# Optimization experiments

Hardware: AMD Instinct MI355X
Metric: run time of the kernel (lower is better)

The kernel has to match this reference:

```python
import jax, jax.numpy as jnp
import numpy as np

B, S, D, H = 4, 2048, 1024, 16
DEPTH = D // H
NEG = float(-2**32 + 1)


def setup_inputs() -> dict:
    key = jax.random.key(0)
    ks = jax.random.split(key, 9)
    std = 1.0 / np.sqrt(D)
    return {
        "q": jax.random.normal(ks[0], (B, S, D), jnp.float32),
        "k": jax.random.normal(ks[1], (B, S, D), jnp.float32),
        "v": jax.random.normal(ks[2], (B, S, D), jnp.float32),
        "Wq": jax.random.normal(ks[3], (D, D), jnp.float32) * std,
        "bq": jnp.zeros((D,), jnp.float32),
        "Wk": jax.random.normal(ks[4], (D, D), jnp.float32) * std,
        "bk": jnp.zeros((D,), jnp.float32),
        "Wv": jax.random.normal(ks[5], (D, D), jnp.float32) * std,
        "bv": jnp.zeros((D,), jnp.float32),
    }


def _split_heads(x):
    # (B,S,D) -> head-major (H*B, S, depth), matching tf stack-on-axis0
    return x.reshape(B, S, H, DEPTH).transpose(2, 0, 1, 3).reshape(H * B, S, DEPTH)


def _merge_heads(x):
    # (H*B, S, depth) -> (B, S, D), heads concatenated on feature dim
    return x.reshape(H, B, S, DEPTH).transpose(1, 2, 0, 3).reshape(B, S, D)


def _attention(qh, kh, vh):
    scale = 1.0 / jnp.sqrt(jnp.float32(DEPTH))
    scores = jnp.einsum("nsd,ntd->nst", qh, kh) * scale  # (N,S,S)
    key_mask = jnp.sign(jnp.abs(jnp.sum(kh, axis=-1)))    # (N,S)
    scores = jnp.where(key_mask[:, None, :] == 0, NEG, scores)
    tril = jnp.tril(jnp.ones((S, S), jnp.float32))
    scores = jnp.where(tril[None] == 0, NEG, scores)
    attn = jax.nn.softmax(scores, axis=-1)
    query_mask = jnp.sign(jnp.abs(jnp.sum(qh, axis=-1)))   # (N,S)
    attn = attn * query_mask[:, :, None]
    return jnp.einsum("nst,ntd->nsd", attn, vh)


def reference(q, k, v, Wq, bq, Wk, bk, Wv, bv):
    qh = _split_heads(q @ Wq + bq)
    kh = _split_heads(k @ Wk + bk)
    vh = _split_heads(v @ Wv + bv)
    out = _attention(qh, kh, vh)
    return _merge_heads(out)
```

## Files before the change

kernel.cpp:

```cpp
#include <hip/hip_runtime.h>

#define S_LEN   2048
#define D_MODEL 1024
#define NB      4
#define NH      16
#define DEP     64
#define NHEADS  64
#define M_ROWS  8192

typedef __bf16 bf16_t;
typedef bf16_t bf16x8 __attribute__((ext_vector_type(8)));
typedef bf16_t bf16x2 __attribute__((ext_vector_type(2)));
typedef float  f32x4  __attribute__((ext_vector_type(4)));
typedef float  f32x16 __attribute__((ext_vector_type(16)));
typedef unsigned int u32x4 __attribute__((ext_vector_type(4)));

#define LOG2E 1.4426950408889634f
#define QSCALE 0.18033688011112043f

#if __has_builtin(__builtin_amdgcn_exp2f)
  #define EXP2(x) __builtin_amdgcn_exp2f(x)
#else
  #define EXP2(x) exp2f(x)
#endif

#define GLOBAL_AS(p) ((const __attribute__((address_space(1))) void*)(p))
#define LDS_AS(p)    ((__attribute__((address_space(3))) void*)(p))

__device__ __forceinline__ unsigned short bf16r(float f) {
  unsigned u = __builtin_bit_cast(unsigned, f);
  u = (u + 0x7FFFu + ((u >> 16) & 1u)) >> 16;
  return (unsigned short)u;
}

__device__ __forceinline__ unsigned pkbf(float lo, float hi) {
  bf16x2 t;
  t[0] = (bf16_t)lo;
  t[1] = (bf16_t)hi;
  return __builtin_bit_cast(unsigned, t);
}

__device__ __forceinline__ bf16x8 exppack8(
    float a0, float a1, float a2, float a3,
    float a4, float a5, float a6, float a7, float& ssum) {
  float e0 = EXP2(a0);
  float e1 = EXP2(a1);
  float e2 = EXP2(a2);
  float e3 = EXP2(a3);
  float e4 = EXP2(a4);
  float e5 = EXP2(a5);
  float e6 = EXP2(a6);
  float e7 = EXP2(a7);
  ssum += ((e0 + e1) + (e2 + e3)) + ((e4 + e5) + (e6 + e7));
  u32x4 fw = {pkbf(e0, e1), pkbf(e2, e3), pkbf(e4, e5), pkbf(e6, e7)};
  return __builtin_bit_cast(bf16x8, fw);
}

__global__ __launch_bounds__(256) void transpose_cvt_w3(
    const float* __restrict__ Wq, const float* __restrict__ Wk,
    const float* __restrict__ Wv,
    unsigned short* __restrict__ oq, unsigned short* __restrict__ ok,
    unsigned short* __restrict__ ov) {
  __shared__ unsigned short tile[32][33];
  int z = blockIdx.z;
  const float* in = (z == 0) ? Wq : (z == 1) ? Wk : Wv;
  unsigned short* out = (z == 0) ? oq : (z == 1) ? ok : ov;
  int bx = blockIdx.x * 32;
  int by = blockIdx.y * 32;
  int tx = threadIdx.x & 31, ty = threadIdx.x >> 5;
  for (int i = ty; i < 32; i += 8)
    tile[i][tx] = bf16r(in[(by + i) * D_MODEL + bx + tx]);
  __syncthreads();
  for (int i = ty; i < 32; i += 8)
    out[(size_t)(bx + i) * D_MODEL + by + tx] = tile[tx][i];
}

__global__ __launch_bounds__(256, 3) void gemm_qkv3(
    const float* __restrict__ Aq, const float* __restrict__ Ak,
    const float* __restrict__ Av,
    const unsigned short* __restrict__ Btq, const unsigned short* __restrict__ Btk,
    const unsigned short* __restrict__ Btv,
    const float* __restrict__ bq, const float* __restrict__ bk,
    const float* __restrict__ bv,
    unsigned short* __restrict__ oq, unsigned short* __restrict__ ok,
    unsigned short* __restrict__ ov) {
  __shared__ __align__(16) float          Asb[128 * 64];
  __shared__ __align__(16) unsigned short Bsb[128 * 64];
  int z = blockIdx.z;
  const float* A           = (z == 0) ? Aq  : (z == 1) ? Ak  : Av;
  const unsigned short* Bt = (z == 0) ? Btq : (z == 1) ? Btk : Btv;
  const float* bias        = (z == 0) ? bq  : (z == 1) ? bk  : bv;
  unsigned short* out      = (z == 0) ? oq  : (z == 1) ? ok  : ov;
  const float scale        = (z == 0) ? QSCALE : 1.0f;
  int tid = threadIdx.x, lane = tid & 63, wid = tid >> 6;
  int lr = lane & 15, lg = lane >> 4;
  int m0 = blockIdx.x * 128, n0 = blockIdx.y * 128;
  int wr = wid >> 1, wc = wid & 1;
  f32x4 acc[4][4] = {};
  for (int kt = 0; kt < D_MODEL / 64; kt++) {
    int k0 = kt * 64;
    if (kt) __syncthreads();
#pragma unroll
    for (int i = 0; i < 8; i++) {
      int chunk = i * 256 + tid;
      int row = chunk >> 4, c = chunk & 15;
      int csrc = c ^ (row & 7);
      __builtin_amdgcn_global_load_lds(
          GLOBAL_AS(A + (size_t)(m0 + row) * D_MODEL + k0 + csrc * 4),
          LDS_AS(Asb + (size_t)(i * 256 + wid * 64) * 4), 16, 0, 0);
    }
#pragma unroll
    for (int i = 0; i < 4; i++) {
      int chunk = i * 256 + tid;
      int r = chunk >> 3, c = chunk & 7;
      int csrc = c ^ (r & 7);
      __builtin_amdgcn_global_load_lds(
          GLOBAL_AS(Bt + (size_t)(n0 + r) * D_MODEL + k0 + csrc * 8),
          LDS_AS(Bsb + (size_t)(i * 256 + wid * 64) * 8), 16, 0, 0);
    }
    __syncthreads();
#pragma unroll
    for (int ks = 0; ks < 2; ks++) {
      bf16x8 af[4], bfr[4];
#pragma unroll
      for (int mi = 0; mi < 4; mi++) {
        int row = wr * 64 + mi * 16 + lr;
        int c0 = (ks * 8 + lg * 2) ^ (row & 7);
        int c1 = (ks * 8 + lg * 2 + 1) ^ (row & 7);
        f32x4 a0 = *(const f32x4*)(Asb + row * 64 + c0 * 4);
        f32x4 a1 = *(const f32x4*)(Asb + row * 64 + c1 * 4);
        u32x4 w = {pkbf(a0[0], a0[1]), pkbf(a0[2], a0[3]),
                   pkbf(a1[0], a1[1]), pkbf(a1[2], a1[3])};
        af[mi] = __builtin_bit_cast(bf16x8, w);
      }
#pragma unroll
      for (int ni = 0; ni < 4; ni++) {
        int row = wc * 64 + ni * 16 + lr;
        int c = (ks * 4 + lg) ^ (row & 7);
        bfr[ni] = *(const bf16x8*)(Bsb + row * 64 + c * 8);
      }
#pragma unroll
      for (int mi = 0; mi < 4; mi++)
#pragma unroll
        for (int ni = 0; ni < 4; ni++)
          acc[mi][ni] = __builtin_amdgcn_mfma_f32_16x16x32_bf16(
              af[mi], bfr[ni], acc[mi][ni], 0, 0, 0);
    }
  }
  if (z != 2) {
#pragma unroll
    for (int mi = 0; mi < 4; mi++) {
#pragma unroll
      for (int ni = 0; ni < 4; ni++) {
        int col = n0 + wc * 64 + ni * 16 + lr;
        float bvv = bias[col];
        int h = col >> 6, d = col & 63;
#pragma unroll
        for (int r = 0; r < 4; r++) {
          int row = m0 + wr * 64 + mi * 16 + lg * 4 + r;
          int b = row >> 11, s = row & (S_LEN - 1);
          float val = (acc[mi][ni][r] + bvv) * scale;
          out[((size_t)(h * NB + b) * S_LEN + s) * DEP + d] = bf16r(val);
        }
      }
    }
  } else {
    int sadj_off = (lg == 1) ? 4 : (lg == 2) ? -4 : 0;
#pragma unroll
    for (int mi = 0; mi < 4; mi++) {
#pragma unroll
      for (int ni = 0; ni < 4; ni++) {
        int col = n0 + wc * 64 + ni * 16 + lr;
        float bvv = bias[col];
        int row0 = m0 + wr * 64 + mi * 16 + lg * 4;
        int b = row0 >> 11, s = (row0 & (S_LEN - 1)) + sadj_off;
        ushort4 w;
        w.x = bf16r(acc[mi][ni][0] + bvv);
        w.y = bf16r(acc[mi][ni][1] + bvv);
        w.z = bf16r(acc[mi][ni][2] + bvv);
        w.w = bf16r(acc[mi][ni][3] + bvv);
        *(ushort4*)(out + ((size_t)((col >> 6) * NB + b) * DEP + (col & 63)) * S_LEN + s) = w;
      }
    }
  }
}

__global__ __launch_bounds__(256, 2) void attn_fwd(
    const unsigned short* __restrict__ Q,
    const unsigned short* __restrict__ K,
    const unsigned short* __restrict__ Vt,
    float* __restrict__ out) {
  __shared__ __align__(16) char smem[65536];
  const int tid = threadIdx.x, lane = tid & 63, wid = tid >> 6;
  const int l31 = lane & 31, hi = lane >> 5;
  const int id = blockIdx.x;
  const int xcd = id & 7, hh = (id >> 3) & 7, u = id >> 6;
  const int n = xcd * 8 + hh;
  const int h = n >> 2, b = n & 3;
  const unsigned short* Qh = Q + (size_t)n * S_LEN * DEP;
  const unsigned short* Kh = K + (size_t)n * S_LEN * DEP;
  const unsigned short* Vh = Vt + (size_t)n * DEP * S_LEN;
  const int S31 = (l31 & 7) << 4;
  const int scol = ((lane & 7) ^ (lane >> 3)) * 8;
  const int srow = lane >> 3;

#define STAGE_TILE(kvb, bi)                                                   \
  {                                                                           \
    char* base_ = smem + (bi) * 16384;                                        \
    const unsigned short* ksrc =                                              \
        Kh + (size_t)((kvb) + wid * 16 + srow) * DEP + scol;                  \
    const unsigned short* vsrc =                                              \
        Vh + (size_t)(wid * 16 + srow) * S_LEN + (kvb) + scol;                \
    unsigned short* kdst = (unsigned short*)base_ + wid * 16 * 64;            \
    unsigned short* vdst = (unsigned short*)(base_ + 8192) + wid * 16 * 64;   \
    __builtin_amdgcn_global_load_lds(GLOBAL_AS(ksrc), LDS_AS(kdst), 16, 0, 0);\
    __builtin_amdgcn_global_load_lds(GLOBAL_AS(ksrc + 8 * DEP),               \
                                     LDS_AS(kdst + 8 * 64), 16, 0, 0);        \
    __builtin_amdgcn_global_load_lds(GLOBAL_AS(vsrc), LDS_AS(vdst), 16, 0, 0);\
    __builtin_amdgcn_global_load_lds(GLOBAL_AS(vsrc + 8 * S_LEN),             \
                                     LDS_AS(vdst + 8 * 64), 16, 0, 0);        \
  }

  for (int pass = 0; pass < 2; ++pass) {
    const int j = pass ? 63 - (u * 4 + wid) : u * 4 + wid;
    const int nt_w = (j >> 1) + 1;
    const int nt_blk = pass ? 32 - 2 * u : 2 * u + 2;
    const int q0 = j * 32;
    const int qrow = q0 + l31;

    bf16x8 qf[4];
#pragma unroll
    for (int ds = 0; ds < 4; ds++)
      qf[ds] = *(const bf16x8*)(Qh + (size_t)qrow * DEP + ds * 16 + hi * 8);

    f32x16 o0 = {}, o1 = {};
    float l = 0.f;

    __syncthreads();
    STAGE_TILE(0, 0);
    STAGE_TILE(64, 1);

    for (int t = 0; t < nt_blk; ++t) {
      if (t + 2 < nt_blk) {
        STAGE_TILE((t + 2) * 64, (t + 2) & 3);
        asm volatile("s_waitcnt vmcnt(8)" ::: "memory");
      } else if (t + 1 < nt_blk) {
        asm volatile("s_waitcnt vmcnt(4)" ::: "memory");
      } else {
        asm volatile("s_waitcnt vmcnt(0)" ::: "memory");
      }
      __builtin_amdgcn_s_barrier();
      asm volatile("" ::: "memory");
      if (t < nt_w) {
        const char* kb = smem + (t & 3) * 16384;
        const char* vb = kb + 8192;
        const int kvb = t * 64;
        const bool diag = (t == nt_w - 1);
        float ssum = 0.f;

        {
          f32x16 p0 = {};
          __builtin_amdgcn_s_setprio(1);
#pragma unroll
          for (int ds = 0; ds < 4; ds++) {
            int off = (ds * 32 + hi * 16) ^ S31;
            bf16x8 kf = *(const bf16x8*)(kb + l31 * 128 + off);
            p0 = __builtin_amdgcn_mfma_f32_32x32x16_bf16(kf, qf[ds], p0, 0, 0, 0);
          }
          __builtin_amdgcn_s_setprio(0);
          if (diag) {
#pragma unroll
            for (int r = 0; r < 16; r++) {
              int kvr = kvb + (r & 3) + 8 * (r >> 2) + 4 * hi;
              if (kvr > qrow) p0[r] = -3.0e38f;
            }
          }
          bf16x8 pa0 = exppack8(p0[0], p0[1], p0[2], p0[3],
                                p0[4], p0[5], p0[6], p0[7], ssum);
          bf16x8 pa1 = exppack8(p0[8], p0[9], p0[10], p0[11],
                                p0[12], p0[13], p0[14], p0[15], ssum);
          __builtin_amdgcn_s_setprio(1);
          {
            int off0 = (0 * 32 + hi * 16) ^ S31;
            int off1 = (1 * 32 + hi * 16) ^ S31;
            bf16x8 vfa = *(const bf16x8*)(vb + l31 * 128 + off0);
            bf16x8 vfb = *(const bf16x8*)(vb + (l31 + 32) * 128 + off0);
            o0 = __builtin_amdgcn_mfma_f32_32x32x16_bf16(vfa, pa0, o0, 0, 0, 0);
            o1 = __builtin_amdgcn_mfma_f32_32x32x16_bf16(vfb, pa0, o1, 0, 0, 0);
            bf16x8 vfc = *(const bf16x8*)(vb + l31 * 128 + off1);
            bf16x8 vfd = *(const bf16x8*)(vb + (l31 + 32) * 128 + off1);
            o0 = __builtin_amdgcn_mfma_f32_32x32x16_bf16(vfc, pa1, o0, 0, 0, 0);
            o1 = __builtin_amdgcn_mfma_f32_32x32x16_bf16(vfd, pa1, o1, 0, 0, 0);
          }
          __builtin_amdgcn_s_setprio(0);
        }
        {
          f32x16 p1 = {};
          __builtin_amdgcn_s_setprio(1);
#pragma unroll
          for (int ds = 0; ds < 4; ds++) {
            int off = (ds * 32 + hi * 16) ^ S31;
            bf16x8 kf = *(const bf16x8*)(kb + (l31 + 32) * 128 + off);
            p1 = __builtin_amdgcn_mfma_f32_32x32x16_bf16(kf, qf[ds], p1, 0, 0, 0);
          }
          __builtin_amdgcn_s_setprio(0);
          if (diag) {
#pragma unroll
            for (int r = 0; r < 16; r++) {
              int kvr = kvb + 32 + (r & 3) + 8 * (r >> 2) + 4 * hi;
              if (kvr > qrow) p1[r] = -3.0e38f;
            }
          }
          bf16x8 pa2 = exppack8(p1[0], p1[1], p1[2], p1[3],
                                p1[4], p1[5], p1[6], p1[7], ssum);
          bf16x8 pa3 = exppack8(p1[8], p1[9], p1[10], p1[11],
                                p1[12], p1[13], p1[14], p1[15], ssum);
          __builtin_amdgcn_s_setprio(1);
          {
            int off0 = (2 * 32 + hi * 16) ^ S31;
            int off1 = (3 * 32 + hi * 16) ^ S31;
            bf16x8 vfa = *(const bf16x8*)(vb + l31 * 128 + off0);
            bf16x8 vfb = *(const bf16x8*)(vb + (l31 + 32) * 128 + off0);
            o0 = __builtin_amdgcn_mfma_f32_32x32x16_bf16(vfa, pa2, o0, 0, 0, 0);
            o1 = __builtin_amdgcn_mfma_f32_32x32x16_bf16(vfb, pa2, o1, 0, 0, 0);
            bf16x8 vfc = *(const bf16x8*)(vb + l31 * 128 + off1);
            bf16x8 vfd = *(const bf16x8*)(vb + (l31 + 32) * 128 + off1);
            o0 = __builtin_amdgcn_mfma_f32_32x32x16_bf16(vfc, pa3, o0, 0, 0, 0);
            o1 = __builtin_amdgcn_mfma_f32_32x32x16_bf16(vfd, pa3, o1, 0, 0, 0);
          }
          __builtin_amdgcn_s_setprio(0);
        }
        ssum += __shfl_xor(ssum, 32);
        l += ssum;
      }
    }
    __syncthreads();

    const float inv = 1.0f / l;
    float* ow = (float*)(smem + wid * 8192);
    const int es = (l31 & 7) << 2;
#pragma unroll
    for (int r = 0; r < 16; r++) {
      int d0 = (r & 3) + 8 * (r >> 2) + 4 * hi;
      ow[l31 * 64 + (d0 ^ es)]        = o0[r] * inv;
      ow[l31 * 64 + ((d0 + 32) ^ es)] = o1[r] * inv;
    }
    asm volatile("s_waitcnt lgkmcnt(0)" ::: "memory");
    __builtin_amdgcn_sched_barrier(0);
#pragma unroll
    for (int i = 0; i < 8; i++) {
      int idx = i * 64 + lane;
      int row = idx >> 4;
      int c4 = idx & 15;
      float4 vv = *(const float4*)&ow[row * 64 + ((c4 * 4) ^ ((row & 7) << 2))];
      *(float4*)(out + (size_t)(b * S_LEN + q0 + row) * D_MODEL + h * DEP + c4 * 4) = vv;
    }
  }
#undef STAGE_TILE
}

extern "C" void kernel_launch(void* const* d_in, const int* in_sizes, int n_in,
                              void* d_out, int out_size, void* d_ws, size_t ws_size,
                              hipStream_t stream) {
  const float* q  = (const float*)d_in[0];
  const float* k  = (const float*)d_in[1];
  const float* v  = (const float*)d_in[2];
  const float* Wq = (const float*)d_in[3];
  const float* bq = (const float*)d_in[4];
  const float* Wk = (const float*)d_in[5];
  const float* bk = (const float*)d_in[6];
  const float* Wv = (const float*)d_in[7];
  const float* bv = (const float*)d_in[8];
  float* out = (float*)d_out;

  const size_t WN = (size_t)D_MODEL * D_MODEL;
  const size_t HN = (size_t)NHEADS * S_LEN * DEP;

  unsigned short* Qh  = (unsigned short*)d_ws;
  unsigned short* Kh  = Qh + HN;
  unsigned short* Vts = Kh + HN;
  unsigned short* Wqt = Vts + HN;
  unsigned short* Wkt = Wqt + WN;
  unsigned short* Wvt = Wkt + WN;

  transpose_cvt_w3<<<dim3(32, 32, 3), 256, 0, stream>>>(Wq, Wk, Wv, Wqt, Wkt, Wvt);

  gemm_qkv3<<<dim3(M_ROWS / 128, D_MODEL / 128, 3), 256, 0, stream>>>(
      q, k, v, Wqt, Wkt, Wvt, bq, bk, bv, Qh, Kh, Vts);

  attn_fwd<<<1024, 256, 0, stream>>>(Qh, Kh, Vts, out);
}
```

Baseline: 175.0 us.

## Process 64 query rows per wave to reuse staged K/V tiles

Each wave now handles two 32-row query sub-blocks (64 rows) instead of one, so every K and V fragment read from LDS feeds twice as many MFMAs. The grid is halved to 512 blocks and the causal diagonal handling skips the fully masked quarter. The aim is to cut LDS read traffic and staging overhead per unit of work. In exchange it raises register pressure (two Q fragment sets and four accumulators), which may lower occupancy, and leaves fewer blocks for load balancing.

```diff
diff --git a/kernel.cpp b/kernel.cpp
--- a/kernel.cpp
+++ b/kernel.cpp
@@ -221,20 +221,84 @@
                                      LDS_AS(vdst + 8 * 64), 16, 0, 0);        \
   }
 
+#define DO_HALF(KROW, VKS, qfv, o0v, o1v, ssumv, qrowv, domask)               \
+  {                                                                           \
+    f32x16 p = {};                                                            \
+    __builtin_amdgcn_s_setprio(1);                                            \
+    _Pragma("unroll")                                                         \
+    for (int ds = 0; ds < 4; ds++) {                                          \
+      int off = (ds * 32 + hi * 16) ^ S31;                                    \
+      bf16x8 kf = *(const bf16x8*)(kb + (l31 + (KROW)) * 128 + off);          \
+      p = __builtin_amdgcn_mfma_f32_32x32x16_bf16(kf, qfv[ds], p, 0, 0, 0);   \
+    }                                                                         \
+    __builtin_amdgcn_s_setprio(0);                                            \
+    if (domask) {                                                             \
+      _Pragma("unroll")                                                       \
+      for (int r = 0; r < 16; r++) {                                          \
+        int kvr = kvb + (KROW) + (r & 3) + 8 * (r >> 2) + 4 * hi;             \
+        if (kvr > (qrowv)) p[r] = -3.0e38f;                                   \
+      }                                                                       \
+    }                                                                         \
+    bf16x8 paA_ = exppack8(p[0], p[1], p[2], p[3],                            \
+                           p[4], p[5], p[6], p[7], ssumv);                    \
+    bf16x8 paB_ = exppack8(p[8], p[9], p[10], p[11],                          \
+                           p[12], p[13], p[14], p[15], ssumv);                \
+    __builtin_amdgcn_s_setprio(1);                                            \
+    {                                                                         \
+      int off0 = ((VKS) * 32 + hi * 16) ^ S31;                                \
+      int off1 = (((VKS) + 1) * 32 + hi * 16) ^ S31;                          \
+      bf16x8 vfa = *(const bf16x8*)(vb + l31 * 128 + off0);                   \
+      bf16x8 vfb = *(const bf16x8*)(vb + (l31 + 32) * 128 + off0);            \
+      o0v = __builtin_amdgcn_mfma_f32_32x32x16_bf16(vfa, paA_, o0v, 0, 0, 0); \
+      o1v = __builtin_amdgcn_mfma_f32_32x32x16_bf16(vfb, paA_, o1v, 0, 0, 0); \
+      bf16x8 vfc = *(const bf16x8*)(vb + l31 * 128 + off1);                   \
+      bf16x8 vfd = *(const bf16x8*)(vb + (l31 + 32) * 128 + off1);            \
+      o0v = __builtin_amdgcn_mfma_f32_32x32x16_bf16(vfc, paB_, o0v, 0, 0, 0); \
+      o1v = __builtin_amdgcn_mfma_f32_32x32x16_bf16(vfd, paB_, o1v, 0, 0, 0); \
+    }                                                                         \
+    __builtin_amdgcn_s_setprio(0);                                            \
+  }
+
+#define EPILOGUE(o0v, o1v, lv, q0v)                                           \
+  {                                                                           \
+    const float inv = 1.0f / (lv);                                            \
+    float* ow = (float*)(smem + wid * 8192);                                  \
+    const int es = (l31 & 7) << 2;                                            \
+    _Pragma("unroll")                                                         \
+    for (int r = 0; r < 16; r++) {                                            \
+      int d0 = (r & 3) + 8 * (r >> 2) + 4 * hi;                               \
+      ow[l31 * 64 + (d0 ^ es)]        = o0v[r] * inv;                         \
+      ow[l31 * 64 + ((d0 + 32) ^ es)] = o1v[r] * inv;                         \
+    }                                                                         \
+    asm volatile("s_waitcnt lgkmcnt(0)" ::: "memory");                        \
+    __builtin_amdgcn_sched_barrier(0);                                        \
+    _Pragma("unroll")                                                         \
+    for (int i = 0; i < 8; i++) {                                             \
+      int idx = i * 64 + lane;                                                \
+      int row = idx >> 4;                                                     \
+      int c4 = idx & 15;                                                      \
+      float4 vv = *(const float4*)&ow[row * 64 + ((c4 * 4) ^ ((row & 7) << 2))]; \
+      *(float4*)(out + (size_t)(b * S_LEN + (q0v) + row) * D_MODEL + h * DEP + c4 * 4) = vv; \
+    }                                                                         \
+  }
+
   for (int pass = 0; pass < 2; ++pass) {
-    const int j = pass ? 63 - (u * 4 + wid) : u * 4 + wid;
-    const int nt_w = (j >> 1) + 1;
-    const int nt_blk = pass ? 32 - 2 * u : 2 * u + 2;
-    const int q0 = j * 32;
-    const int qrow = q0 + l31;
-
-    bf16x8 qf[4];
-#pragma unroll
-    for (int ds = 0; ds < 4; ds++)
-      qf[ds] = *(const bf16x8*)(Qh + (size_t)qrow * DEP + ds * 16 + hi * 8);
-
-    f32x16 o0 = {}, o1 = {};
-    float l = 0.f;
+    const int m = pass ? 31 - (u * 4 + wid) : u * 4 + wid;
+    const int nt_w = m + 1;
+    const int nt_blk = pass ? 32 - 4 * u : 4 * u + 4;
+    const int q0 = m * 64;
+    const int qrowA = q0 + l31;
+    const int qrowB = q0 + 32 + l31;
+
+    bf16x8 qfA[4], qfB[4];
+#pragma unroll
+    for (int ds = 0; ds < 4; ds++) {
+      qfA[ds] = *(const bf16x8*)(Qh + (size_t)qrowA * DEP + ds * 16 + hi * 8);
+      qfB[ds] = *(const bf16x8*)(Qh + (size_t)qrowB * DEP + ds * 16 + hi * 8);
+    }
+
+    f32x16 oA0 = {}, oA1 = {}, oB0 = {}, oB1 = {};
+    float lA = 0.f, lB = 0.f;
 
     __syncthreads();
     STAGE_TILE(0, 0);
@@ -256,107 +320,30 @@
         const char* vb = kb + 8192;
         const int kvb = t * 64;
         const bool diag = (t == nt_w - 1);
-        float ssum = 0.f;
-
-        {
-          f32x16 p0 = {};
-          __builtin_amdgcn_s_setprio(1);
-#pragma unroll
-          for (int ds = 0; ds < 4; ds++) {
-            int off = (ds * 32 + hi * 16) ^ S31;
-            bf16x8 kf = *(const bf16x8*)(kb + l31 * 128 + off);
-            p0 = __builtin_amdgcn_mfma_f32_32x32x16_bf16(kf, qf[ds], p0, 0, 0, 0);
-          }
-          __builtin_amdgcn_s_setprio(0);
-          if (diag) {
-#pragma unroll
-            for (int r = 0; r < 16; r++) {
-              int kvr = kvb + (r & 3) + 8 * (r >> 2) + 4 * hi;
-              if (kvr > qrow) p0[r] = -3.0e38f;
-            }
-          }
-          bf16x8 pa0 = exppack8(p0[0], p0[1], p0[2], p0[3],
-                                p0[4], p0[5], p0[6], p0[7], ssum);
-          bf16x8 pa1 = exppack8(p0[8], p0[9], p0[10], p0[11],
-                                p0[12], p0[13], p0[14], p0[15], ssum);
-          __builtin_amdgcn_s_setprio(1);
-          {
-            int off0 = (0 * 32 + hi * 16) ^ S31;
-            int off1 = (1 * 32 + hi * 16) ^ S31;
-            bf16x8 vfa = *(const bf16x8*)(vb + l31 * 128 + off0);
-            bf16x8 vfb = *(const bf16x8*)(vb + (l31 + 32) * 128 + off0);
-            o0 = __builtin_amdgcn_mfma_f32_32x32x16_bf16(vfa, pa0, o0, 0, 0, 0);
-            o1 = __builtin_amdgcn_mfma_f32_32x32x16_bf16(vfb, pa0, o1, 0, 0, 0);
-            bf16x8 vfc = *(const bf16x8*)(vb + l31 * 128 + off1);
-            bf16x8 vfd = *(const bf16x8*)(vb + (l31 + 32) * 128 + off1);
-            o0 = __builtin_amdgcn_mfma_f32_32x32x16_bf16(vfc, pa1, o0, 0, 0, 0);
-            o1 = __builtin_amdgcn_mfma_f32_32x32x16_bf16(vfd, pa1, o1, 0, 0, 0);
-          }
-          __builtin_amdgcn_s_setprio(0);
+        float ssumA = 0.f, ssumB = 0.f;
+
+        DO_HALF(0, 0, qfA, oA0, oA1, ssumA, qrowA, diag);
+        DO_HALF(0, 0, qfB, oB0, oB1, ssumB, qrowB, 0);
+        if (!diag) {
+          DO_HALF(32, 2, qfA, oA0, oA1, ssumA, qrowA, 0);
         }
-        {
-          f32x16 p1 = {};
-          __builtin_amdgcn_s_setprio(1);
-#pragma unroll
-          for (int ds = 0; ds < 4; ds++) {
-            int off = (ds * 32 + hi * 16) ^ S31;
-            bf16x8 kf = *(const bf16x8*)(kb + (l31 + 32) * 128 + off);
-            p1 = __builtin_amdgcn_mfma_f32_32x32x16_bf16(kf, qf[ds], p1, 0, 0, 0);
-          }
-          __builtin_amdgcn_s_setprio(0);
-          if (diag) {
-#pragma unroll
-            for (int r = 0; r < 16; r++) {
-              int kvr = kvb + 32 + (r & 3) + 8 * (r >> 2) + 4 * hi;
-              if (kvr > qrow) p1[r] = -3.0e38f;
-            }
-          }
-          bf16x8 pa2 = exppack8(p1[0], p1[1], p1[2], p1[3],
-                                p1[4], p1[5], p1[6], p1[7], ssum);
-          bf16x8 pa3 = exppack8(p1[8], p1[9], p1[10], p1[11],
-                                p1[12], p1[13], p1[14], p1[15], ssum);
-          __builtin_amdgcn_s_setprio(1);
-          {
-            int off0 = (2 * 32 + hi * 16) ^ S31;
-            int off1 = (3 * 32 + hi * 16) ^ S31;
-            bf16x8 vfa = *(const bf16x8*)(vb + l31 * 128 + off0);
-            bf16x8 vfb = *(const bf16x8*)(vb + (l31 + 32) * 128 + off0);
-            o0 = __builtin_amdgcn_mfma_f32_32x32x16_bf16(vfa, pa2, o0, 0, 0, 0);
-            o1 = __builtin_amdgcn_mfma_f32_32x32x16_bf16(vfb, pa2, o1, 0, 0, 0);
-            bf16x8 vfc = *(const bf16x8*)(vb + l31 * 128 + off1);
-            bf16x8 vfd = *(const bf16x8*)(vb + (l31 + 32) * 128 + off1);
-            o0 = __builtin_amdgcn_mfma_f32_32x32x16_bf16(vfc, pa3, o0, 0, 0, 0);
-            o1 = __builtin_amdgcn_mfma_f32_32x32x16_bf16(vfd, pa3, o1, 0, 0, 0);
-          }
-          __builtin_amdgcn_s_setprio(0);
-        }
-        ssum += __shfl_xor(ssum, 32);
-        l += ssum;
+        DO_HALF(32, 2, qfB, oB0, oB1, ssumB, qrowB, diag);
+
+        ssumA += __shfl_xor(ssumA, 32);
+        lA += ssumA;
+        ssumB += __shfl_xor(ssumB, 32);
+        lB += ssumB;
       }
     }
     __syncthreads();
 
-    const float inv = 1.0f / l;
-    float* ow = (float*)(smem + wid * 8192);
-    const int es = (l31 & 7) << 2;
-#pragma unroll
-    for (int r = 0; r < 16; r++) {
-      int d0 = (r & 3) + 8 * (r >> 2) + 4 * hi;
-      ow[l31 * 64 + (d0 ^ es)]        = o0[r] * inv;
-      ow[l31 * 64 + ((d0 + 32) ^ es)] = o1[r] * inv;
-    }
+    EPILOGUE(oA0, oA1, lA, q0);
     asm volatile("s_waitcnt lgkmcnt(0)" ::: "memory");
-    __builtin_amdgcn_sched_barrier(0);
-#pragma unroll
-    for (int i = 0; i < 8; i++) {
-      int idx = i * 64 + lane;
-      int row = idx >> 4;
-      int c4 = idx & 15;
-      float4 vv = *(const float4*)&ow[row * 64 + ((c4 * 4) ^ ((row & 7) << 2))];
-      *(float4*)(out + (size_t)(b * S_LEN + q0 + row) * D_MODEL + h * DEP + c4 * 4) = vv;
-    }
+    EPILOGUE(oB0, oB1, lB, q0 + 32);
   }
 #undef STAGE_TILE
+#undef DO_HALF
+#undef EPILOGUE
 }
 
 extern "C" void kernel_launch(void* const* d_in, const int* in_sizes, int n_in,
@@ -388,5 +375,5 @@
   gemm_qkv3<<<dim3(M_ROWS / 128, D_MODEL / 128, 3), 256, 0, stream>>>(
       q, k, v, Wqt, Wkt, Wvt, bq, bk, bv, Qh, Kh, Vts);
 
-  attn_fwd<<<1024, 256, 0, stream>>>(Qh, Kh, Vts, out);
-}
+  attn_fwd<<<512, 256, 0, stream>>>(Qh, Kh, Vts, out);
+}
```

Measured after the change: 167.6 us (median of 2 runs). 1.04x faster.
